# Optimization experiments

Hardware: AMD Instinct MI355X
Metric: run time of the kernel (lower is better)

## Reference

```python
import jax, jax.numpy as jnp
import numpy as np


def setup_inputs() -> dict:
    key = jax.random.key(0)
    k1, k2, k3 = jax.random.split(key, 3)
    B, N, D, T = 8, 2, 256, 500
    SPK = 2000
    H = jax.random.normal(k1, (B, N, D, T), dtype=jnp.float32)
    S = jax.random.randint(k2, (B, N, T), 0, SPK, dtype=jnp.int64)
    E = jax.random.normal(k3, (SPK, D), dtype=jnp.float32)
    alpha = jnp.ones((1,), dtype=jnp.float32) * 10.0
    beta = jnp.ones((1,), dtype=jnp.float32) * 5.0
    return {"H": H, "S": S, "E": E, "alpha": alpha, "beta": beta, "N": 2}


def reference(H, S, E, alpha, beta, N):
    # H: (B, N, D, T); S: (B, N, T) int ids; E: (SPK, D)
    B, N_, D, T = H.shape
    # embedding lookup: (B, N, T, D) -> (B, N, D, T)
    E_S = jnp.transpose(E[S], (0, 1, 3, 2))
    # pairwise dist between predicted vectors and active-speaker embeddings
    # (B, N_pred=N, N_emb=N, T) -- small, direct broadcast
    Dist_p = jnp.sum((H[:, None, :, :, :] - E_S[:, :, None, :, :]) ** 2, axis=3)
    # N == 2 path matching (identity vs swap), min over the two alignments
    p0 = Dist_p[:, 0, 0, :] + Dist_p[:, 1, 1, :]  # (B, T)
    p1 = Dist_p[:, 0, 1, :] + Dist_p[:, 1, 0, :]  # (B, T)
    Dmin = jnp.minimum(p0, p1)                    # (B, T)
    Dmin = -alpha * Dmin + beta                   # broadcast (1,) over (B, T)
    # full distance to every speaker: ||H||^2 + ||E||^2 - 2 H.E
    # avoids materializing (B, SPK, N, D, T)
    Hsq = jnp.sum(H * H, axis=2)                  # (B, N, T)
    Esq = jnp.sum(E * E, axis=1)                  # (SPK,)
    cross = jnp.einsum('bndt,sd->bsnt', H, E)     # (B, SPK, N, T)
    Dist = Hsq[:, None, :, :] + Esq[None, :, None, None] - 2.0 * cross
    Dist = -alpha * Dist + beta                   # (B, SPK, N, T)
    lse = jax.nn.logsumexp(Dist, axis=1)          # (B, N, T)
    loss = -jnp.mean(Dmin) + jnp.mean(lse)
    return (E_S[:, :, :, 0], loss)
```

## Files before the change

kernel.cpp:

```cpp
#include <hip/hip_runtime.h>
#include <math.h>

#define Bb   8
#define Dd   256
#define Tt   500
#define SPK  2000
#define SPKP 2048
#define BN   16
#define L2E  1.4426950408889634f
#define LN2  0.6931471805599453f

#define EXP2F(x) __builtin_amdgcn_exp2f(x)
#define LOG2F(x) __builtin_amdgcn_logf(x)

#define F_ESN   0
#define F_DMINP 2048
#define F_HSQP  4096
#define F_PM    36864
#define F_PL    69632
#define EBF_BYTES ((size_t)102400 * 4)
#define HBF_BYTES (EBF_BYTES + (size_t)1048576)

typedef __bf16 v8bf __attribute__((ext_vector_type(8)));
typedef float  v4f  __attribute__((ext_vector_type(4)));

__device__ inline unsigned pack_bf16x2(float lo, float hi) {
    union { __bf16 h; unsigned short u; } a, b;
    a.h = (__bf16)lo; b.h = (__bf16)hi;
    return ((unsigned)b.u << 16) | (unsigned)a.u;
}

__global__ __launch_bounds__(256) void prep_all_kernel(
        const float* __restrict__ E, const int* __restrict__ S,
        const float* __restrict__ H, const float* __restrict__ alpha,
        const float* __restrict__ beta, float* __restrict__ ws,
        float* __restrict__ out) {
    int bid = blockIdx.x;
    int tid = threadIdx.x;

    if (bid < 512) {
        int s = bid * 4 + (tid >> 6);
        int lane = tid & 63;
        float4 v = make_float4(0.f, 0.f, 0.f, 0.f);
        if (s < SPK) v = ((const float4*)E)[s * 64 + lane];
        __bf16* ebf = (__bf16*)((char*)ws + EBF_BYTES);
        uint2 pp;
        pp.x = pack_bf16x2(v.x, v.y);
        pp.y = pack_bf16x2(v.z, v.w);
        *(uint2*)(ebf + (size_t)s * Dd + lane * 4) = pp;
        float acc = v.x * v.x + v.y * v.y + v.z * v.z + v.w * v.w;
        #pragma unroll
        for (int off = 32; off > 0; off >>= 1) acc += __shfl_down(acc, off, 64);
        if (lane == 0) ws[F_ESN + s] = (s < SPK) ? (-alpha[0] * acc * L2E) : -1e30f;
    } else if (bid < 528) {
        int i = (bid - 512) * 256 + tid;
        int bn = i >> 8, d = i & 255;
        out[i] = E[(size_t)S[bn * Tt] * Dd + d];
    } else if (bid < 656) {
        __shared__ float4 shm[8][32];
        int qq = bid - 528;
        int b = qq >> 4;
        int t0 = (qq & 15) * 32;
        int tl = tid & 31;
        int wv = tid >> 5;
        int t = t0 + tl;
        bool ok = (t < Tt);
        int tc = ok ? t : (Tt - 1);
        int s0 = S[(b * 2 + 0) * Tt + tc];
        int s1 = S[(b * 2 + 1) * Tt + tc];
        const float* h0 = H + ((size_t)(b * 2 + 0) * Dd) * Tt + tc;
        const float* h1 = H + ((size_t)(b * 2 + 1) * Dd) * Tt + tc;
        const float* e0 = E + (size_t)s0 * Dd;
        const float* e1 = E + (size_t)s1 * Dd;
        float d00 = 0, d01 = 0, d10 = 0, d11 = 0;
        int dbase = wv * 32;
        #pragma unroll 4
        for (int dd = 0; dd < 32; ++dd) {
            int d = dbase + dd;
            float x0 = h0[(size_t)d * Tt], x1 = h1[(size_t)d * Tt];
            float y0 = e0[d], y1 = e1[d];
            float u;
            u = x0 - y0; d00 = fmaf(u, u, d00);
            u = x0 - y1; d01 = fmaf(u, u, d01);
            u = x1 - y0; d10 = fmaf(u, u, d10);
            u = x1 - y1; d11 = fmaf(u, u, d11);
        }
        shm[wv][tl] = make_float4(d00, d01, d10, d11);
        __syncthreads();
        if (tid < 32) {
            d00 = 0; d01 = 0; d10 = 0; d11 = 0;
            #pragma unroll
            for (int g = 0; g < 8; ++g) {
                float4 p = shm[g][tl];
                d00 += p.x; d01 += p.y; d10 += p.z; d11 += p.w;
            }
            float dm = fminf(d00 + d11, d01 + d10);
            float val = ok ? (-alpha[0] * dm + beta[0]) : 0.f;
            #pragma unroll
            for (int off = 16; off > 0; off >>= 1) val += __shfl_down(val, off, 32);
            if (tid == 0) ws[F_DMINP + qq] = val;
        }
    } else {
        __shared__ float trans[32][65];
        int u = bid - 656;
        int bn = u >> 6;
        int r = u & 63;
        int tt0 = (r & 15) * 32;
        int d0 = (r >> 4) * 64;
        const float* Hb = H + (size_t)bn * Dd * Tt;
        #pragma unroll
        for (int p = 0; p < 8; ++p) {
            int flat = p * 256 + tid;
            int dd = flat >> 5;
            int tl = flat & 31;
            int t = tt0 + tl;
            trans[tl][dd] = (t < Tt) ? Hb[(size_t)(d0 + dd) * Tt + t] : 0.f;
        }
        __syncthreads();
        int tw = tid >> 3;
        int j = tid & 7;
        float sq = 0.f;
        float vals[8];
        #pragma unroll
        for (int e = 0; e < 8; ++e) {
            float x = trans[tw][j * 8 + e];
            vals[e] = x;
            sq = fmaf(x, x, sq);
        }
        sq += __shfl_xor(sq, 1, 64);
        sq += __shfl_xor(sq, 2, 64);
        sq += __shfl_xor(sq, 4, 64);
        uint4 pk;
        pk.x = pack_bf16x2(vals[0], vals[1]);
        pk.y = pack_bf16x2(vals[2], vals[3]);
        pk.z = pack_bf16x2(vals[4], vals[5]);
        pk.w = pack_bf16x2(vals[6], vals[7]);
        __bf16* hbf = (__bf16*)((char*)ws + HBF_BYTES);
        *(uint4*)(hbf + ((size_t)(bn * 512 + tt0 + tw) * Dd + d0 + j * 8)) = pk;
        if (j == 0) ws[F_HSQP + (size_t)(bn * 512 + tt0 + tw) * 4 + (r >> 4)] = sq;
    }
}

__global__ __launch_bounds__(256, 2) void lse_mfma_kernel(
        const float* __restrict__ alpha, const float* __restrict__ beta,
        float* __restrict__ ws) {
    __shared__ __bf16 shB[64 * 264];
    __shared__ __bf16 shA[64 * 264];
    __shared__ float mrg_m[4][4][16], mrg_l[4][4][16];

    int bn = blockIdx.x;
    int t0 = blockIdx.y * 64;
    int mz = blockIdx.z;
    int tid = threadIdx.x;
    int lane = tid & 63;
    int n = lane & 15;
    int q = lane >> 4;
    int w = tid >> 6;

    const __bf16* ebf = (const __bf16*)((const char*)ws + EBF_BYTES);
    const __bf16* hbf = (const __bf16*)((const char*)ws + HBF_BYTES);

    #pragma unroll
    for (int p = 0; p < 8; ++p) {
        int flat = p * 256 + tid;
        int row = flat >> 5;
        int ch = flat & 31;
        uint4 v = *(const uint4*)(hbf + ((size_t)(bn * 512 + t0 + row) * Dd + ch * 8));
        *(uint4*)(shB + row * 264 + ch * 8) = v;
    }
    __syncthreads();

    v8bf bq[4][8];
    #pragma unroll
    for (int i = 0; i < 4; ++i) {
        int tloc = 16 * i + n;
        #pragma unroll
        for (int ks = 0; ks < 8; ++ks) {
            bq[i][ks] = *reinterpret_cast<const v8bf*>(&shB[tloc * 264 + ks * 32 + q * 8]);
        }
    }

    float A = alpha[0], Bv = beta[0];
    float ta2p = 2.f * A * L2E;
    float ctc2[4];
    #pragma unroll
    for (int i = 0; i < 4; ++i) {
        int t = t0 + 16 * i + n;
        float4 hq = *(const float4*)(ws + F_HSQP + (size_t)(bn * 512 + t) * 4);
        float hs = hq.x + hq.y + hq.z + hq.w;
        ctc2[i] = (t < Tt) ? ((Bv - A * hs) * L2E) : 0.f;
    }

    float lm[4], ll[4];
    #pragma unroll
    for (int i = 0; i < 4; ++i) { lm[i] = -INFINITY; ll[i] = 0.f; }

    for (int c = 0; c < 8; ++c) {
        int sbase = mz * 512 + c * 64;
        __syncthreads();
        #pragma unroll
        for (int p = 0; p < 8; ++p) {
            int flat = p * 256 + tid;
            int row = flat >> 5;
            int ch = flat & 31;
            uint4 v = *(const uint4*)(ebf + ((size_t)(sbase + row) * Dd + ch * 8));
            *(uint4*)(shA + row * 264 + ch * 8) = v;
        }
        __syncthreads();

        int sb = sbase + w * 16;
        v8bf af[8];
        #pragma unroll
        for (int ks = 0; ks < 8; ++ks) {
            af[ks] = *reinterpret_cast<const v8bf*>(&shA[(w * 16 + n) * 264 + ks * 32 + q * 8]);
        }
        float4 es4 = *(const float4*)(ws + F_ESN + sb + q * 4);

        v4f acc[4];
        #pragma unroll
        for (int i = 0; i < 4; ++i) acc[i] = (v4f){0.f, 0.f, 0.f, 0.f};
        #pragma unroll
        for (int ks = 0; ks < 8; ++ks) {
            #pragma unroll
            for (int i = 0; i < 4; ++i) {
                acc[i] = __builtin_amdgcn_mfma_f32_16x16x32_bf16(af[ks], bq[i][ks], acc[i], 0, 0, 0);
            }
        }
        float e0 = es4.x, e1 = es4.y, e2 = es4.z, e3 = es4.w;
        #pragma unroll
        for (int i = 0; i < 4; ++i) {
            float c2 = ctc2[i];
            float v0 = fmaf(ta2p, acc[i][0], c2 + e0);
            float v1 = fmaf(ta2p, acc[i][1], c2 + e1);
            float v2 = fmaf(ta2p, acc[i][2], c2 + e2);
            float v3 = fmaf(ta2p, acc[i][3], c2 + e3);
            float vm = fmaxf(fmaxf(v0, v1), fmaxf(v2, v3));
            float s = EXP2F(v0 - vm) + EXP2F(v1 - vm) + EXP2F(v2 - vm) + EXP2F(v3 - vm);
            float nm = fmaxf(lm[i], vm);
            ll[i] = ll[i] * EXP2F(lm[i] - nm) + s * EXP2F(vm - nm);
            lm[i] = nm;
        }
    }

    #pragma unroll
    for (int i = 0; i < 4; ++i) {
        float m = lm[i], l = ll[i];
        #pragma unroll
        for (int msk = 16; msk <= 32; msk <<= 1) {
            float om = __shfl_xor(m, msk, 64);
            float ol = __shfl_xor(l, msk, 64);
            float nm = fmaxf(m, om);
            l = l * EXP2F(m - nm) + ol * EXP2F(om - nm);
            m = nm;
        }
        if (q == 0) { mrg_m[w][i][n] = m; mrg_l[w][i][n] = l; }
    }
    __syncthreads();

    if (tid < 64) {
        int i = tid >> 4, cc = tid & 15;
        float m = mrg_m[0][i][cc], l = mrg_l[0][i][cc];
        #pragma unroll
        for (int wv = 1; wv < 4; ++wv) {
            float om = mrg_m[wv][i][cc], ol = mrg_l[wv][i][cc];
            float nm = fmaxf(m, om);
            l = l * EXP2F(m - nm) + ol * EXP2F(om - nm);
            m = nm;
        }
        int tw = t0 + 16 * i + cc;
        if (tw < Tt) {
            ws[F_PM + (bn * 512 + tw) * 4 + mz] = m;
            ws[F_PL + (bn * 512 + tw) * 4 + mz] = l;
        }
    }
}

__global__ __launch_bounds__(1024) void final_kernel(const float* __restrict__ ws,
                                                     float* __restrict__ out) {
    __shared__ float rL[16], rD[16];
    int tid = threadIdx.x;
    float lsum = 0.f;
    #pragma unroll
    for (int it = 0; it < 8; ++it) {
        int idx = it * 1024 + tid;
        int bn = idx >> 9, t = idx & 511;
        if (t < Tt) {
            int base = (bn * 512 + t) * 4;
            float m = ws[F_PM + base], l = ws[F_PL + base];
            #pragma unroll
            for (int s = 1; s < 4; ++s) {
                float om = ws[F_PM + base + s], ol = ws[F_PL + base + s];
                float nm = fmaxf(m, om);
                l = l * EXP2F(m - nm) + ol * EXP2F(om - nm);
                m = nm;
            }
            lsum += LN2 * (m + LOG2F(l));
        }
    }
    float dsum = (tid < 128) ? ws[F_DMINP + tid] : 0.f;
    #pragma unroll
    for (int off = 32; off > 0; off >>= 1) {
        lsum += __shfl_down(lsum, off, 64);
        dsum += __shfl_down(dsum, off, 64);
    }
    if ((tid & 63) == 0) { rL[tid >> 6] = lsum; rD[tid >> 6] = dsum; }
    __syncthreads();
    if (tid == 0) {
        float L = 0.f, D = 0.f;
        #pragma unroll
        for (int wv = 0; wv < 16; ++wv) { L += rL[wv]; D += rD[wv]; }
        out[BN * Dd] = -(D / (float)(Bb * Tt)) + L / (float)(BN * Tt);
    }
}

extern "C" void kernel_launch(void* const* d_in, const int* in_sizes, int n_in,
                              void* d_out, int out_size, void* d_ws, size_t ws_size,
                              hipStream_t stream) {
    const float* H     = (const float*)d_in[0];
    const int*   S     = (const int*)d_in[1];
    const float* E     = (const float*)d_in[2];
    const float* alpha = (const float*)d_in[3];
    const float* beta  = (const float*)d_in[4];
    float* out = (float*)d_out;
    float* ws  = (float*)d_ws;

    prep_all_kernel<<<1680, 256, 0, stream>>>(E, S, H, alpha, beta, ws, out);
    lse_mfma_kernel<<<dim3(BN, 8, 4), 256, 0, stream>>>(alpha, beta, ws);
    final_kernel<<<1, 1024, 0, stream>>>(ws, out);
}
```

Measured before the change: 102.1 us.

## Swizzle bf16 layouts, use direct global-to-LDS loads, fuse final reduction via last-block counter

The prep kernel now writes the bf16 E and H tiles with an XOR swizzle, so the MFMA kernel can fill shared memory with global_load_lds 16-byte transfers instead of load-then-store through registers. The padded LDS rows are dropped in favour of the swizzle to avoid bank conflicts. The separate final reduction kernel is removed: a global atomic counter elects the last block to do the cross-split logsumexp merge and write the loss, which saves one launch. In exchange the code now relies on threadfence ordering and on the counter reset done in the prep kernel.

```diff
diff --git a/kernel.cpp b/kernel.cpp
--- a/kernel.cpp
+++ b/kernel.cpp
@@ -15,6 +15,7 @@
 
 #define F_ESN   0
 #define F_DMINP 2048
+#define F_CNT   2176
 #define F_HSQP  4096
 #define F_PM    36864
 #define F_PL    69632
@@ -23,6 +24,13 @@
 
 typedef __bf16 v8bf __attribute__((ext_vector_type(8)));
 typedef float  v4f  __attribute__((ext_vector_type(4)));
+
+typedef const __attribute__((address_space(1))) unsigned int as1_u32;
+typedef __attribute__((address_space(3))) unsigned int as3_u32;
+
+__device__ __forceinline__ void gload_lds16(const void* g, void* l) {
+    __builtin_amdgcn_global_load_lds((as1_u32*)g, (as3_u32*)l, 16, 0, 0);
+}
 
 __device__ inline unsigned pack_bf16x2(float lo, float hi) {
     union { __bf16 h; unsigned short u; } a, b;
@@ -39,15 +47,16 @@
     int tid = threadIdx.x;
 
     if (bid < 512) {
+        if (bid == 0 && tid == 0) ((unsigned*)ws)[F_CNT] = 0u;
         int s = bid * 4 + (tid >> 6);
         int lane = tid & 63;
         float4 v = make_float4(0.f, 0.f, 0.f, 0.f);
         if (s < SPK) v = ((const float4*)E)[s * 64 + lane];
-        __bf16* ebf = (__bf16*)((char*)ws + EBF_BYTES);
         uint2 pp;
         pp.x = pack_bf16x2(v.x, v.y);
         pp.y = pack_bf16x2(v.z, v.w);
-        *(uint2*)(ebf + (size_t)s * Dd + lane * 4) = pp;
+        int xo = (lane * 8) ^ ((s & 7) << 4);
+        *(uint2*)((char*)ws + EBF_BYTES + (size_t)s * 512 + xo) = pp;
         float acc = v.x * v.x + v.y * v.y + v.z * v.z + v.w * v.w;
         #pragma unroll
         for (int off = 32; off > 0; off >>= 1) acc += __shfl_down(acc, off, 64);
@@ -135,18 +144,21 @@
         pk.y = pack_bf16x2(vals[2], vals[3]);
         pk.z = pack_bf16x2(vals[4], vals[5]);
         pk.w = pack_bf16x2(vals[6], vals[7]);
-        __bf16* hbf = (__bf16*)((char*)ws + HBF_BYTES);
-        *(uint4*)(hbf + ((size_t)(bn * 512 + tt0 + tw) * Dd + d0 + j * 8)) = pk;
-        if (j == 0) ws[F_HSQP + (size_t)(bn * 512 + tt0 + tw) * 4 + (r >> 4)] = sq;
+        int row = tt0 + tw;
+        int xo = (d0 * 2 + j * 16) ^ ((row & 7) << 4);
+        *(uint4*)((char*)ws + HBF_BYTES + (size_t)(bn * 512 + row) * 512 + xo) = pk;
+        if (j == 0) ws[F_HSQP + (size_t)(bn * 512 + row) * 4 + (r >> 4)] = sq;
     }
 }
 
 __global__ __launch_bounds__(256, 2) void lse_mfma_kernel(
         const float* __restrict__ alpha, const float* __restrict__ beta,
-        float* __restrict__ ws) {
-    __shared__ __bf16 shB[64 * 264];
-    __shared__ __bf16 shA[64 * 264];
+        float* __restrict__ ws, float* __restrict__ out) {
+    __shared__ __bf16 shB[64 * 256];
+    __shared__ __bf16 shA[64 * 256];
     __shared__ float mrg_m[4][4][16], mrg_l[4][4][16];
+    __shared__ unsigned sflag;
+    __shared__ float rL[4], rD[4];
 
     int bn = blockIdx.x;
     int t0 = blockIdx.y * 64;
@@ -157,26 +169,28 @@
     int q = lane >> 4;
     int w = tid >> 6;
 
-    const __bf16* ebf = (const __bf16*)((const char*)ws + EBF_BYTES);
-    const __bf16* hbf = (const __bf16*)((const char*)ws + HBF_BYTES);
-
-    #pragma unroll
-    for (int p = 0; p < 8; ++p) {
-        int flat = p * 256 + tid;
-        int row = flat >> 5;
-        int ch = flat & 31;
-        uint4 v = *(const uint4*)(hbf + ((size_t)(bn * 512 + t0 + row) * Dd + ch * 8));
-        *(uint4*)(shB + row * 264 + ch * 8) = v;
+    const char* ebf = (const char*)ws + EBF_BYTES;
+    const char* hbf = (const char*)ws + HBF_BYTES;
+
+    {
+        const char* src = hbf + (size_t)(bn * 512 + t0) * 512;
+        #pragma unroll
+        for (int p = 0; p < 8; ++p) {
+            int o = p * 4096 + w * 1024;
+            gload_lds16(src + o + lane * 16, (char*)shB + o);
+        }
     }
     __syncthreads();
 
     v8bf bq[4][8];
     #pragma unroll
     for (int i = 0; i < 4; ++i) {
-        int tloc = 16 * i + n;
+        int r = 16 * i + n;
+        int swz = (r & 7) << 4;
         #pragma unroll
         for (int ks = 0; ks < 8; ++ks) {
-            bq[i][ks] = *reinterpret_cast<const v8bf*>(&shB[tloc * 264 + ks * 32 + q * 8]);
+            bq[i][ks] = *reinterpret_cast<const v8bf*>(
+                (const char*)shB + r * 512 + ((ks * 64 + q * 16) ^ swz));
         }
     }
 
@@ -195,26 +209,27 @@
     #pragma unroll
     for (int i = 0; i < 4; ++i) { lm[i] = -INFINITY; ll[i] = 0.f; }
 
+    int ra = w * 16 + n;
+    int swzA = (ra & 7) << 4;
+
     for (int c = 0; c < 8; ++c) {
         int sbase = mz * 512 + c * 64;
         __syncthreads();
+        const char* srcA = ebf + (size_t)sbase * 512;
         #pragma unroll
         for (int p = 0; p < 8; ++p) {
-            int flat = p * 256 + tid;
-            int row = flat >> 5;
-            int ch = flat & 31;
-            uint4 v = *(const uint4*)(ebf + ((size_t)(sbase + row) * Dd + ch * 8));
-            *(uint4*)(shA + row * 264 + ch * 8) = v;
+            int o = p * 4096 + w * 1024;
+            gload_lds16(srcA + o + lane * 16, (char*)shA + o);
         }
         __syncthreads();
 
-        int sb = sbase + w * 16;
         v8bf af[8];
         #pragma unroll
         for (int ks = 0; ks < 8; ++ks) {
-            af[ks] = *reinterpret_cast<const v8bf*>(&shA[(w * 16 + n) * 264 + ks * 32 + q * 8]);
-        }
-        float4 es4 = *(const float4*)(ws + F_ESN + sb + q * 4);
+            af[ks] = *reinterpret_cast<const v8bf*>(
+                (const char*)shA + ra * 512 + ((ks * 64 + q * 16) ^ swzA));
+        }
+        float4 es4 = *(const float4*)(ws + F_ESN + sbase + w * 16 + q * 4);
 
         v4f acc[4];
         #pragma unroll
@@ -273,27 +288,29 @@
             ws[F_PL + (bn * 512 + tw) * 4 + mz] = l;
         }
     }
-}
-
-__global__ __launch_bounds__(1024) void final_kernel(const float* __restrict__ ws,
-                                                     float* __restrict__ out) {
-    __shared__ float rL[16], rD[16];
-    int tid = threadIdx.x;
+
+    __threadfence();
+    __syncthreads();
+    if (tid == 0) {
+        unsigned old = atomicAdd((unsigned*)ws + F_CNT, 1u);
+        sflag = (old == 511u);
+    }
+    __syncthreads();
+    if (!sflag) return;
+    __threadfence();
+
     float lsum = 0.f;
     #pragma unroll
-    for (int it = 0; it < 8; ++it) {
-        int idx = it * 1024 + tid;
-        int bn = idx >> 9, t = idx & 511;
+    for (int it = 0; it < 32; ++it) {
+        int idx = it * 256 + tid;
+        int t = idx & 511;
         if (t < Tt) {
-            int base = (bn * 512 + t) * 4;
-            float m = ws[F_PM + base], l = ws[F_PL + base];
-            #pragma unroll
-            for (int s = 1; s < 4; ++s) {
-                float om = ws[F_PM + base + s], ol = ws[F_PL + base + s];
-                float nm = fmaxf(m, om);
-                l = l * EXP2F(m - nm) + ol * EXP2F(om - nm);
-                m = nm;
-            }
+            float4 m4 = *(const float4*)(ws + F_PM + idx * 4);
+            float4 l4 = *(const float4*)(ws + F_PL + idx * 4);
+            float m = m4.x, l = l4.x, nm;
+            nm = fmaxf(m, m4.y); l = l * EXP2F(m - nm) + l4.y * EXP2F(m4.y - nm); m = nm;
+            nm = fmaxf(m, m4.z); l = l * EXP2F(m - nm) + l4.z * EXP2F(m4.z - nm); m = nm;
+            nm = fmaxf(m, m4.w); l = l * EXP2F(m - nm) + l4.w * EXP2F(m4.w - nm); m = nm;
             lsum += LN2 * (m + LOG2F(l));
         }
     }
@@ -303,12 +320,11 @@
         lsum += __shfl_down(lsum, off, 64);
         dsum += __shfl_down(dsum, off, 64);
     }
-    if ((tid & 63) == 0) { rL[tid >> 6] = lsum; rD[tid >> 6] = dsum; }
+    if (lane == 0) { rL[w] = lsum; rD[w] = dsum; }
     __syncthreads();
     if (tid == 0) {
-        float L = 0.f, D = 0.f;
-        #pragma unroll
-        for (int wv = 0; wv < 16; ++wv) { L += rL[wv]; D += rD[wv]; }
+        float L = rL[0] + rL[1] + rL[2] + rL[3];
+        float D = rD[0] + rD[1] + rD[2] + rD[3];
         out[BN * Dd] = -(D / (float)(Bb * Tt)) + L / (float)(BN * Tt);
     }
 }
@@ -325,6 +341,5 @@
     float* ws  = (float*)d_ws;
 
     prep_all_kernel<<<1680, 256, 0, stream>>>(E, S, H, alpha, beta, ws, out);
-    lse_mfma_kernel<<<dim3(BN, 8, 4), 256, 0, stream>>>(alpha, beta, ws);
-    final_kernel<<<1, 1024, 0, stream>>>(ws, out);
-}
+    lse_mfma_kernel<<<dim3(BN, 8, 4), 256, 0, stream>>>(alpha, beta, ws, out);
+}
```

Measured after the change: 143.0 us. 1.4x slower.

## Fuse final reduction into LSE kernel via last-block atomic; prefetch E tiles into registers

Applied to the files above, without the earlier changes.

Removes the separate final_kernel launch. Each LSE block bumps an atomic counter, and the last block to finish merges the partial max/sum pairs and writes the loss, using vectorized float4 reads. The E-tile loads are also double-buffered through registers, so the next tile's global load overlaps the MFMA work on the current one. This saves one launch and its gap at the cost of serial tail work in a single 256-thread block, extra register pressure, and fences.

```diff
diff --git a/kernel.cpp b/kernel.cpp
--- a/kernel.cpp
+++ b/kernel.cpp
@@ -15,6 +15,7 @@
 
 #define F_ESN   0
 #define F_DMINP 2048
+#define F_CNT   2176
 #define F_HSQP  4096
 #define F_PM    36864
 #define F_PL    69632
@@ -39,6 +40,7 @@
     int tid = threadIdx.x;
 
     if (bid < 512) {
+        if (bid == 0 && tid == 0) ((unsigned*)ws)[F_CNT] = 0u;
         int s = bid * 4 + (tid >> 6);
         int lane = tid & 63;
         float4 v = make_float4(0.f, 0.f, 0.f, 0.f);
@@ -143,10 +145,12 @@
 
 __global__ __launch_bounds__(256, 2) void lse_mfma_kernel(
         const float* __restrict__ alpha, const float* __restrict__ beta,
-        float* __restrict__ ws) {
+        float* __restrict__ ws, float* __restrict__ out) {
     __shared__ __bf16 shB[64 * 264];
     __shared__ __bf16 shA[64 * 264];
     __shared__ float mrg_m[4][4][16], mrg_l[4][4][16];
+    __shared__ unsigned sflag;
+    __shared__ float rL[4], rD[4];
 
     int bn = blockIdx.x;
     int t0 = blockIdx.y * 64;
@@ -160,6 +164,8 @@
     const __bf16* ebf = (const __bf16*)((const char*)ws + EBF_BYTES);
     const __bf16* hbf = (const __bf16*)((const char*)ws + HBF_BYTES);
 
+    int flat_row = tid >> 2;
+
     #pragma unroll
     for (int p = 0; p < 8; ++p) {
         int flat = p * 256 + tid;
@@ -195,18 +201,40 @@
     #pragma unroll
     for (int i = 0; i < 4; ++i) { lm[i] = -INFINITY; ll[i] = 0.f; }
 
-    for (int c = 0; c < 8; ++c) {
-        int sbase = mz * 512 + c * 64;
-        __syncthreads();
+    uint4 rg[8];
+    {
+        int sbase = mz * 512;
         #pragma unroll
         for (int p = 0; p < 8; ++p) {
             int flat = p * 256 + tid;
             int row = flat >> 5;
             int ch = flat & 31;
-            uint4 v = *(const uint4*)(ebf + ((size_t)(sbase + row) * Dd + ch * 8));
-            *(uint4*)(shA + row * 264 + ch * 8) = v;
-        }
+            rg[p] = *(const uint4*)(ebf + ((size_t)(sbase + row) * Dd + ch * 8));
+        }
+    }
+
+    for (int c = 0; c < 8; ++c) {
+        int sbase = mz * 512 + c * 64;
         __syncthreads();
+        #pragma unroll
+        for (int p = 0; p < 8; ++p) {
+            int flat = p * 256 + tid;
+            int row = flat >> 5;
+            int ch = flat & 31;
+            *(uint4*)(shA + row * 264 + ch * 8) = rg[p];
+        }
+        __syncthreads();
+
+        if (c < 7) {
+            int nbase = sbase + 64;
+            #pragma unroll
+            for (int p = 0; p < 8; ++p) {
+                int flat = p * 256 + tid;
+                int row = flat >> 5;
+                int ch = flat & 31;
+                rg[p] = *(const uint4*)(ebf + ((size_t)(nbase + row) * Dd + ch * 8));
+            }
+        }
 
         int sb = sbase + w * 16;
         v8bf af[8];
@@ -273,27 +301,29 @@
             ws[F_PL + (bn * 512 + tw) * 4 + mz] = l;
         }
     }
-}
-
-__global__ __launch_bounds__(1024) void final_kernel(const float* __restrict__ ws,
-                                                     float* __restrict__ out) {
-    __shared__ float rL[16], rD[16];
-    int tid = threadIdx.x;
+
+    __threadfence();
+    __syncthreads();
+    if (tid == 0) {
+        unsigned old = atomicAdd((unsigned*)ws + F_CNT, 1u);
+        sflag = (old == 511u);
+    }
+    __syncthreads();
+    if (!sflag) return;
+    __threadfence();
+
     float lsum = 0.f;
     #pragma unroll
-    for (int it = 0; it < 8; ++it) {
-        int idx = it * 1024 + tid;
-        int bn = idx >> 9, t = idx & 511;
+    for (int it = 0; it < 32; ++it) {
+        int idx = it * 256 + tid;
+        int t = idx & 511;
         if (t < Tt) {
-            int base = (bn * 512 + t) * 4;
-            float m = ws[F_PM + base], l = ws[F_PL + base];
-            #pragma unroll
-            for (int s = 1; s < 4; ++s) {
-                float om = ws[F_PM + base + s], ol = ws[F_PL + base + s];
-                float nm = fmaxf(m, om);
-                l = l * EXP2F(m - nm) + ol * EXP2F(om - nm);
-                m = nm;
-            }
+            float4 m4 = *(const float4*)(ws + F_PM + idx * 4);
+            float4 l4 = *(const float4*)(ws + F_PL + idx * 4);
+            float m = m4.x, l = l4.x, nm;
+            nm = fmaxf(m, m4.y); l = l * EXP2F(m - nm) + l4.y * EXP2F(m4.y - nm); m = nm;
+            nm = fmaxf(m, m4.z); l = l * EXP2F(m - nm) + l4.z * EXP2F(m4.z - nm); m = nm;
+            nm = fmaxf(m, m4.w); l = l * EXP2F(m - nm) + l4.w * EXP2F(m4.w - nm); m = nm;
             lsum += LN2 * (m + LOG2F(l));
         }
     }
@@ -303,12 +333,11 @@
         lsum += __shfl_down(lsum, off, 64);
         dsum += __shfl_down(dsum, off, 64);
     }
-    if ((tid & 63) == 0) { rL[tid >> 6] = lsum; rD[tid >> 6] = dsum; }
+    if (lane == 0) { rL[w] = lsum; rD[w] = dsum; }
     __syncthreads();
     if (tid == 0) {
-        float L = 0.f, D = 0.f;
-        #pragma unroll
-        for (int wv = 0; wv < 16; ++wv) { L += rL[wv]; D += rD[wv]; }
+        float L = rL[0] + rL[1] + rL[2] + rL[3];
+        float D = rD[0] + rD[1] + rD[2] + rD[3];
         out[BN * Dd] = -(D / (float)(Bb * Tt)) + L / (float)(BN * Tt);
     }
 }
@@ -325,6 +354,5 @@
     float* ws  = (float*)d_ws;
 
     prep_all_kernel<<<1680, 256, 0, stream>>>(E, S, H, alpha, beta, ws, out);
-    lse_mfma_kernel<<<dim3(BN, 8, 4), 256, 0, stream>>>(alpha, beta, ws);
-    final_kernel<<<1, 1024, 0, stream>>>(ws, out);
+    lse_mfma_kernel<<<dim3(BN, 8, 4), 256, 0, stream>>>(alpha, beta, ws, out);
 }
```

New measurement: 177.9 us. 1.74x slower.
